# Optimization experiments

Hardware: AMD Instinct MI355X
Metric: run time of the kernel (lower is better)

The kernel has to match this reference:

```python
import jax, jax.numpy as jnp
import numpy as np

N_NODES = 50000
N_EDGES = 800000
IN_DIM = 256
NHID = 64
OUT_DIM = 64
DEPTH = 4
P = 2.0


def _gcn_conv(x, W, b, src, dst, n):
    # PyG GCNConv: xW, add self-loops, sym-normalize, aggregate src->dst, + bias
    xw = x @ W
    loop = jnp.arange(n)
    s = jnp.concatenate([src, loop])
    d = jnp.concatenate([dst, loop])
    deg = jax.ops.segment_sum(jnp.ones_like(d, dtype=xw.dtype), d, num_segments=n)
    dis = jnp.where(deg > 0, jax.lax.rsqrt(jnp.maximum(deg, 1.0)), 0.0)
    w = dis[s] * dis[d]  # [E+n]
    out = jax.ops.segment_sum(w[:, None] * xw[s], d, num_segments=n)
    return out + b


def _g2_gate(x, W, b, src, dst, n):
    xg = jax.nn.relu(_gcn_conv(x, W, b, src, dst, n))
    diff = jnp.abs(xg[src] - xg[dst]) ** P  # [E, nhid]
    sums = jax.ops.segment_sum(diff, src, num_segments=n)
    cnt = jax.ops.segment_sum(jnp.ones((src.shape[0],), dtype=x.dtype), src, num_segments=n)
    return jnp.tanh(sums / jnp.maximum(cnt, 1.0)[:, None])


def setup_inputs() -> dict:
    key = jax.random.key(0)
    ks = jax.random.split(key, 10)
    x = jax.random.normal(ks[0], (N_NODES, IN_DIM), dtype=jnp.float32)
    edge_index = jax.random.randint(ks[1], (2, N_EDGES), 0, N_NODES, dtype=jnp.int64 if jax.config.jax_enable_x64 else jnp.int32)
    s = 0.05
    return {
        "x": x,
        "edge_index": edge_index,
        "enc_w": jax.random.normal(ks[2], (IN_DIM, NHID), dtype=jnp.float32) * s,
        "enc_b": jnp.zeros((NHID,), dtype=jnp.float32),
        "conv_w": jax.random.normal(ks[3], (NHID, NHID), dtype=jnp.float32) * s,
        "conv_b": jnp.zeros((NHID,), dtype=jnp.float32),
        "gg_w": jax.random.normal(ks[4], (NHID, NHID), dtype=jnp.float32) * s,
        "gg_b": jnp.zeros((NHID,), dtype=jnp.float32),
        "dec_w": jax.random.normal(ks[5], (NHID, OUT_DIM), dtype=jnp.float32) * s,
        "dec_b": jnp.zeros((OUT_DIM,), dtype=jnp.float32),
    }


def reference(x, edge_index, enc_w, enc_b, conv_w, conv_b, gg_w, gg_b, dec_w, dec_b):
    n = x.shape[0]
    src, dst = edge_index[0], edge_index[1]
    # eval mode: dropouts are identity
    X = jax.nn.relu(x @ enc_w + enc_b)
    for _ in range(DEPTH):
        X_ = jax.nn.relu(_gcn_conv(X, conv_w, conv_b, src, dst, n))
        tau = _g2_gate(X, gg_w, gg_b, src, dst, n)
        X = (1.0 - tau) * X + tau * X_
    X = jax.nn.relu(X @ dec_w + dec_b)
    return X
```

## Files before the change

### kernel.cpp

```cpp
#include <hip/hip_runtime.h>
#include <math.h>

#define NN 50000
#define NE 800000
#define IND 256
#define NH 64
#define DEPTH 4
#define PART_DIV 6250
#define SB 49


__device__ __forceinline__ unsigned short f2bf(float f) {
    unsigned int x = __float_as_uint(f);
    unsigned int r = (x + 0x7fffu + ((x >> 16) & 1u)) >> 16;
    return (unsigned short)r;
}
__device__ __forceinline__ unsigned int pack2bf(float lo, float hi) {
    return (unsigned int)f2bf(lo) | ((unsigned int)f2bf(hi) << 16);
}
__device__ __forceinline__ ushort4 f4_to_us4(float4 f) {
    ushort4 u;
    u.x = f2bf(f.x); u.y = f2bf(f.y); u.z = f2bf(f.z); u.w = f2bf(f.w);
    return u;
}
__device__ __forceinline__ void acc8(float* a, uint4 r) {
    a[0] += __uint_as_float(r.x << 16); a[1] += __uint_as_float(r.x & 0xffff0000u);
    a[2] += __uint_as_float(r.y << 16); a[3] += __uint_as_float(r.y & 0xffff0000u);
    a[4] += __uint_as_float(r.z << 16); a[5] += __uint_as_float(r.z & 0xffff0000u);
    a[6] += __uint_as_float(r.w << 16); a[7] += __uint_as_float(r.w & 0xffff0000u);
}
__device__ __forceinline__ void unpack8(float* a, uint4 r) {
    a[0] = __uint_as_float(r.x << 16); a[1] = __uint_as_float(r.x & 0xffff0000u);
    a[2] = __uint_as_float(r.y << 16); a[3] = __uint_as_float(r.y & 0xffff0000u);
    a[4] = __uint_as_float(r.z << 16); a[5] = __uint_as_float(r.z & 0xffff0000u);
    a[6] = __uint_as_float(r.w << 16); a[7] = __uint_as_float(r.w & 0xffff0000u);
}
__device__ __forceinline__ void accd8(float* a, const float* xg, uint4 r) {
    float e;
    e = xg[0] - __uint_as_float(r.x << 16);         a[0] += e * e;
    e = xg[1] - __uint_as_float(r.x & 0xffff0000u); a[1] += e * e;
    e = xg[2] - __uint_as_float(r.y << 16);         a[2] += e * e;
    e = xg[3] - __uint_as_float(r.y & 0xffff0000u); a[3] += e * e;
    e = xg[4] - __uint_as_float(r.z << 16);         a[4] += e * e;
    e = xg[5] - __uint_as_float(r.z & 0xffff0000u); a[5] += e * e;
    e = xg[6] - __uint_as_float(r.w << 16);         a[6] += e * e;
    e = xg[7] - __uint_as_float(r.w & 0xffff0000u); a[7] += e * e;
}
__device__ __forceinline__ float tanh_pos(float x) {
    float t = __expf(-2.f * x);
    return (1.f - t) / (1.f + t);
}


__global__ void count_deg_rank(const int* __restrict__ src, const int* __restrict__ dst,
                               int* __restrict__ degin, int* __restrict__ degout,
                               int* __restrict__ rank_in, int* __restrict__ rank_out) {
    int e = blockIdx.x * blockDim.x + threadIdx.x;
    if (e < NE) {
        int s = src[e], d = dst[e];
        rank_in[e]  = atomicAdd(&degin[d], 1);
        rank_out[e] = atomicAdd(&degout[s], 1);
    }
}

__global__ __launch_bounds__(512) void scan_p1(const int* __restrict__ in0,
                                               const int* __restrict__ in1,
                                               int* __restrict__ tmp,
                                               int* __restrict__ bsum) {
    int a = blockIdx.x / SB;
    int b = blockIdx.x % SB;
    const int* in = a ? in1 : in0;
    int t = threadIdx.x;
    int base = b * 1024 + t * 2;
    int v0 = (base < NN) ? in[base] : 0;
    int v1 = (base + 1 < NN) ? in[base + 1] : 0;
    int v = v0 + v1;
    int x = v;
#pragma unroll
    for (int off = 1; off < 64; off <<= 1) {
        int u = __shfl_up(x, off);
        if ((t & 63) >= off) x += u;
    }
    __shared__ int ws[8];
    int wid = t >> 6, lane = t & 63;
    if (lane == 63) ws[wid] = x;
    __syncthreads();
    if (t == 0) {
        int run = 0;
#pragma unroll
        for (int w = 0; w < 8; ++w) { int s = ws[w]; ws[w] = run; run += s; }
    }
    __syncthreads();
    x += ws[wid];
    int excl = x - v;
    if (base < NN) tmp[a * NN + base] = excl;
    if (base + 1 < NN) tmp[a * NN + base + 1] = excl + v0;
    if (t == 511) bsum[a * SB + b] = x;
}

__global__ __launch_bounds__(128) void scan_p2(int* __restrict__ bsum,
                                               int* __restrict__ out0,
                                               int* __restrict__ out1) {
    int t = threadIdx.x;
    int a = t >> 6, lane = t & 63;
    int v = (lane < SB) ? bsum[a * SB + lane] : 0;
    int x = v;
#pragma unroll
    for (int off = 1; off < 64; off <<= 1) {
        int u = __shfl_up(x, off);
        if (lane >= off) x += u;
    }
    if (lane < SB) bsum[a * SB + lane] = x - v;
    if (lane == SB - 1) {
        if (a == 0) out0[NN] = x; else out1[NN] = x;
    }
}

__global__ __launch_bounds__(512) void scan_p3(const int* __restrict__ tmp,
                                               const int* __restrict__ bsum,
                                               int* __restrict__ out0,
                                               int* __restrict__ out1) {
    int a = blockIdx.x / SB;
    int b = blockIdx.x % SB;
    int* out = a ? out1 : out0;
    int add = bsum[a * SB + b];
    int t = threadIdx.x;
    int base = b * 1024 + t * 2;
    if (base < NN) out[base] = tmp[a * NN + base] + add;
    if (base + 1 < NN) out[base + 1] = tmp[a * NN + base + 1] + add;
}

__global__ void init_node(const int* __restrict__ degin, const int* __restrict__ degout,
                          float* __restrict__ dis, float* __restrict__ cntf) {
    int i = blockIdx.x * blockDim.x + threadIdx.x;
    if (i < NN) {
        dis[i] = rsqrtf((float)(degin[i] + 1));
        int od = degout[i];
        cntf[i] = (float)(od > 0 ? od : 1);
    }
}

__global__ void fill_csr_part(const int* __restrict__ src, const int* __restrict__ dst,
                              const int* __restrict__ off_dst, const int* __restrict__ off_src,
                              const int* __restrict__ rank_in, const int* __restrict__ rank_out,
                              int* __restrict__ srcs_by_dst, int* __restrict__ dsts_by_src,
                              int nGroups) {
    int p = blockIdx.x & 7;
    int g = blockIdx.x >> 3;
    for (int e = g * 256 + threadIdx.x; e < NE; e += nGroups * 256) {
        int s = src[e], d = dst[e];
        if (d / PART_DIV == p) srcs_by_dst[off_dst[d] + rank_in[e]] = s;
        if (s / PART_DIV == p) dsts_by_src[off_src[s] + rank_out[e]] = d;
    }
}

template<int K, bool RELU, bool WSC>
__global__ __launch_bounds__(256) void gemm64b(const float* __restrict__ X,
                                               const float* __restrict__ W,
                                               const float* __restrict__ bias,
                                               const float* __restrict__ rowscale,
                                               float* __restrict__ out,
                                               unsigned short* __restrict__ xsc, int n) {
    __shared__ float Ws[64 * 64];
    __shared__ float Xs[64][68];
    int tid = threadIdx.x;
    int row0 = blockIdx.x * 64;
    int r16 = tid >> 4;
    int cg = tid & 15;
    float4 acc[4];
#pragma unroll
    for (int t = 0; t < 4; ++t) acc[t] = make_float4(0.f, 0.f, 0.f, 0.f);

    for (int kc = 0; kc < K; kc += 64) {
        const float4* W4 = (const float4*)(W + (size_t)kc * 64);
        float4* Ws4 = (float4*)Ws;
#pragma unroll
        for (int t = 0; t < 4; ++t) Ws4[tid + t * 256] = W4[tid + t * 256];
#pragma unroll
        for (int t = 0; t < 4; ++t) {
            int r = r16 + t * 16;
            int grow = row0 + r;
            float4 xv = make_float4(0.f, 0.f, 0.f, 0.f);
            if (grow < n) xv = *(const float4*)(X + (size_t)grow * K + kc + cg * 4);
            Xs[r][cg * 4 + 0] = xv.x; Xs[r][cg * 4 + 1] = xv.y;
            Xs[r][cg * 4 + 2] = xv.z; Xs[r][cg * 4 + 3] = xv.w;
        }
        __syncthreads();
#pragma unroll
        for (int k = 0; k < 64; ++k) {
            float4 w4 = ((const float4*)Ws)[k * 16 + cg];
#pragma unroll
            for (int t = 0; t < 4; ++t) {
                float xv = Xs[r16 + t * 16][k];
                acc[t].x += xv * w4.x; acc[t].y += xv * w4.y;
                acc[t].z += xv * w4.z; acc[t].w += xv * w4.w;
            }
        }
        __syncthreads();
    }

    float4 b4 = ((const float4*)bias)[cg];
#pragma unroll
    for (int t = 0; t < 4; ++t) {
        int row = row0 + r16 + t * 16;
        if (row < n) {
            float4 o;
            o.x = acc[t].x + b4.x; o.y = acc[t].y + b4.y;
            o.z = acc[t].z + b4.z; o.w = acc[t].w + b4.w;
            if (RELU) {
                o.x = fmaxf(o.x, 0.f); o.y = fmaxf(o.y, 0.f);
                o.z = fmaxf(o.z, 0.f); o.w = fmaxf(o.w, 0.f);
            }
            ((float4*)(out + (size_t)row * 64))[cg] = o;
            if (WSC) {
                float s = rowscale[row];
                float4 o2 = make_float4(o.x * s, o.y * s, o.z * s, o.w * s);
                ((ushort4*)(xsc + (size_t)row * 64))[cg] = f4_to_us4(o2);
            }
        }
    }
}

template<bool OUTBF>
__global__ __launch_bounds__(256) void gemm64z(const float* __restrict__ Z,
                                               const float* __restrict__ W,
                                               const float* __restrict__ bias,
                                               float* __restrict__ outf,
                                               unsigned short* __restrict__ outb, int n) {
    __shared__ float Ws[64 * 64];
    __shared__ float Xs[64][68];
    int tid = threadIdx.x;
    int row0 = blockIdx.x * 64;
    int r16 = tid >> 4;
    int cg = tid & 15;
    float4 acc[4];
#pragma unroll
    for (int t = 0; t < 4; ++t) acc[t] = make_float4(0.f, 0.f, 0.f, 0.f);

    {
        const float4* W4 = (const float4*)W;
        float4* Ws4 = (float4*)Ws;
#pragma unroll
        for (int t = 0; t < 4; ++t) Ws4[tid + t * 256] = W4[tid + t * 256];
#pragma unroll
        for (int t = 0; t < 4; ++t) {
            int r = r16 + t * 16;
            int gr = row0 + r;
            float4 xv = make_float4(0.f, 0.f, 0.f, 0.f);
            if (gr < n) xv = *(const float4*)(Z + (size_t)gr * 64 + cg * 4);
            Xs[r][cg * 4 + 0] = xv.x; Xs[r][cg * 4 + 1] = xv.y;
            Xs[r][cg * 4 + 2] = xv.z; Xs[r][cg * 4 + 3] = xv.w;
        }
        __syncthreads();
#pragma unroll
        for (int k = 0; k < 64; ++k) {
            float4 w4 = ((const float4*)Ws)[k * 16 + cg];
#pragma unroll
            for (int t = 0; t < 4; ++t) {
                float xv = Xs[r16 + t * 16][k];
                acc[t].x += xv * w4.x; acc[t].y += xv * w4.y;
                acc[t].z += xv * w4.z; acc[t].w += xv * w4.w;
            }
        }
    }

    float4 b4 = ((const float4*)bias)[cg];
#pragma unroll
    for (int t = 0; t < 4; ++t) {
        int row = row0 + r16 + t * 16;
        if (row < n) {
            float4 o;
            o.x = fmaxf(acc[t].x + b4.x, 0.f); o.y = fmaxf(acc[t].y + b4.y, 0.f);
            o.z = fmaxf(acc[t].z + b4.z, 0.f); o.w = fmaxf(acc[t].w + b4.w, 0.f);
            if (OUTBF) {
                ((ushort4*)(outb + (size_t)row * 64))[cg] = f4_to_us4(o);
            } else {
                ((float4*)(outf + (size_t)row * 64))[cg] = o;
            }
        }
    }
}

__global__ __launch_bounds__(256) void zgather(
    const unsigned short* __restrict__ Xbf,
    const int* __restrict__ off, const int* __restrict__ nbr,
    const float* __restrict__ dis, float* __restrict__ Z)
{
    int t = blockIdx.x * 256 + threadIdx.x;
    int node = t >> 3, l8 = t & 7;
    if (node >= NN) return;
    const uint4* Xb = (const uint4*)Xbf;
    float a[8];
    unpack8(a, Xb[(size_t)node * 8 + l8]);
    int lo = off[node], hi = off[node + 1];
    int j = lo;
    for (; j + 7 < hi; j += 8) {
        int s0 = nbr[j],     s1 = nbr[j + 1], s2 = nbr[j + 2], s3 = nbr[j + 3];
        int s4 = nbr[j + 4], s5 = nbr[j + 5], s6 = nbr[j + 6], s7 = nbr[j + 7];
        uint4 r0 = Xb[(size_t)s0 * 8 + l8];
        uint4 r1 = Xb[(size_t)s1 * 8 + l8];
        uint4 r2 = Xb[(size_t)s2 * 8 + l8];
        uint4 r3 = Xb[(size_t)s3 * 8 + l8];
        uint4 r4 = Xb[(size_t)s4 * 8 + l8];
        uint4 r5 = Xb[(size_t)s5 * 8 + l8];
        uint4 r6 = Xb[(size_t)s6 * 8 + l8];
        uint4 r7 = Xb[(size_t)s7 * 8 + l8];
        acc8(a, r0); acc8(a, r1); acc8(a, r2); acc8(a, r3);
        acc8(a, r4); acc8(a, r5); acc8(a, r6); acc8(a, r7);
    }
    for (; j + 3 < hi; j += 4) {
        int s0 = nbr[j], s1 = nbr[j + 1], s2 = nbr[j + 2], s3 = nbr[j + 3];
        uint4 r0 = Xb[(size_t)s0 * 8 + l8];
        uint4 r1 = Xb[(size_t)s1 * 8 + l8];
        uint4 r2 = Xb[(size_t)s2 * 8 + l8];
        uint4 r3 = Xb[(size_t)s3 * 8 + l8];
        acc8(a, r0); acc8(a, r1); acc8(a, r2); acc8(a, r3);
    }
    for (; j < hi; ++j) {
        acc8(a, Xb[(size_t)nbr[j] * 8 + l8]);
    }
    float di = dis[node];
    float* zp = Z + (size_t)node * 64 + l8 * 8;
    *(float4*)(zp)     = make_float4(di * a[0], di * a[1], di * a[2], di * a[3]);
    *(float4*)(zp + 4) = make_float4(di * a[4], di * a[5], di * a[6], di * a[7]);
}

__global__ __launch_bounds__(256) void gate_update8(
    const unsigned short* __restrict__ Cbf, const float* __restrict__ Xn,
    float* __restrict__ X, unsigned short* __restrict__ Xbf,
    const int* __restrict__ off, const int* __restrict__ nbr,
    const float* __restrict__ cntf, const float* __restrict__ dis)
{
    int t = blockIdx.x * 256 + threadIdx.x;
    int node = t >> 3, l8 = t & 7;
    if (node >= NN) return;
    const uint4* Cb = (const uint4*)Cbf;
    float xg[8];
    unpack8(xg, Cb[(size_t)node * 8 + l8]);
    float a[8] = {0.f, 0.f, 0.f, 0.f, 0.f, 0.f, 0.f, 0.f};
    int lo = off[node], hi = off[node + 1];
    int j = lo;
    for (; j + 7 < hi; j += 8) {
        int d0 = nbr[j],     d1 = nbr[j + 1], d2 = nbr[j + 2], d3 = nbr[j + 3];
        int d4 = nbr[j + 4], d5 = nbr[j + 5], d6 = nbr[j + 6], d7 = nbr[j + 7];
        uint4 r0 = Cb[(size_t)d0 * 8 + l8];
        uint4 r1 = Cb[(size_t)d1 * 8 + l8];
        uint4 r2 = Cb[(size_t)d2 * 8 + l8];
        uint4 r3 = Cb[(size_t)d3 * 8 + l8];
        uint4 r4 = Cb[(size_t)d4 * 8 + l8];
        uint4 r5 = Cb[(size_t)d5 * 8 + l8];
        uint4 r6 = Cb[(size_t)d6 * 8 + l8];
        uint4 r7 = Cb[(size_t)d7 * 8 + l8];
        accd8(a, xg, r0); accd8(a, xg, r1); accd8(a, xg, r2); accd8(a, xg, r3);
        accd8(a, xg, r4); accd8(a, xg, r5); accd8(a, xg, r6); accd8(a, xg, r7);
    }
    for (; j + 3 < hi; j += 4) {
        int d0 = nbr[j], d1 = nbr[j + 1], d2 = nbr[j + 2], d3 = nbr[j + 3];
        uint4 r0 = Cb[(size_t)d0 * 8 + l8];
        uint4 r1 = Cb[(size_t)d1 * 8 + l8];
        uint4 r2 = Cb[(size_t)d2 * 8 + l8];
        uint4 r3 = Cb[(size_t)d3 * 8 + l8];
        accd8(a, xg, r0); accd8(a, xg, r1); accd8(a, xg, r2); accd8(a, xg, r3);
    }
    for (; j < hi; ++j) {
        accd8(a, xg, Cb[(size_t)nbr[j] * 8 + l8]);
    }
    float inv = 1.f / cntf[node];
    float di = dis[node];
    const float* xop = X + (size_t)node * 64 + l8 * 8;
    const float* xnp = Xn + (size_t)node * 64 + l8 * 8;
    float o[8];
#pragma unroll
    for (int k = 0; k < 8; ++k) {
        float tau = tanh_pos(a[k] * inv);
        float xo = xop[k], xn = xnp[k];
        o[k] = xo + tau * (xn - xo);
    }
    float* xp = X + (size_t)node * 64 + l8 * 8;
    *(float4*)(xp)     = make_float4(o[0], o[1], o[2], o[3]);
    *(float4*)(xp + 4) = make_float4(o[4], o[5], o[6], o[7]);
    uint4 pk;
    pk.x = pack2bf(o[0] * di, o[1] * di);
    pk.y = pack2bf(o[2] * di, o[3] * di);
    pk.z = pack2bf(o[4] * di, o[5] * di);
    pk.w = pack2bf(o[6] * di, o[7] * di);
    ((uint4*)Xbf)[(size_t)node * 8 + l8] = pk;
}


extern "C" void kernel_launch(void* const* d_in, const int* in_sizes, int n_in,
                              void* d_out, int out_size, void* d_ws, size_t ws_size,
                              hipStream_t stream) {
    const float* x      = (const float*)d_in[0];
    const int*   ei     = (const int*)d_in[1];
    const float* enc_w  = (const float*)d_in[2];
    const float* enc_b  = (const float*)d_in[3];
    const float* conv_w = (const float*)d_in[4];
    const float* conv_b = (const float*)d_in[5];
    const float* gg_w   = (const float*)d_in[6];
    const float* gg_b   = (const float*)d_in[7];
    const float* dec_w  = (const float*)d_in[8];
    const float* dec_b  = (const float*)d_in[9];
    float* out = (float*)d_out;

    const int* src = ei;
    const int* dst = ei + NE;

    char* p = (char*)d_ws;
    auto alloc = [&](size_t bytes) -> void* {
        void* r = (void*)p;
        p += (bytes + 255) & ~(size_t)255;
        return r;
    };
    float* X   = (float*)alloc((size_t)NN * 64 * 4);
    float* Zb  = (float*)alloc((size_t)NN * 64 * 4);
    float* B   = (float*)alloc((size_t)NN * 64 * 4);
    unsigned short* Xbf = (unsigned short*)alloc((size_t)NN * 64 * 2);
    unsigned short* Cbf = (unsigned short*)alloc((size_t)NN * 64 * 2);
    float* dis  = (float*)alloc((size_t)NN * 4);
    float* cntf = (float*)alloc((size_t)NN * 4);
    int* degin   = (int*)alloc((size_t)NN * 4);
    int* degout  = (int*)alloc((size_t)NN * 4);
    int* off_dst = (int*)alloc((size_t)(NN + 1) * 4);
    int* off_src = (int*)alloc((size_t)(NN + 1) * 4);
    int* rank_in  = (int*)alloc((size_t)NE * 4);
    int* rank_out = (int*)alloc((size_t)NE * 4);
    int* sbd     = (int*)alloc((size_t)NE * 4);
    int* dbs     = (int*)alloc((size_t)NE * 4);
    int* stmp    = (int*)alloc((size_t)2 * NN * 4);
    int* bsum    = (int*)alloc((size_t)2 * SB * 4);

    hipMemsetAsync(degin, 0, (size_t)NN * 4, stream);
    hipMemsetAsync(degout, 0, (size_t)NN * 4, stream);

    const int EB = (NE + 255) / 256;
    const int NB = (NN + 255) / 256;
    const int NGROUPS = 104;
    count_deg_rank<<<EB, 256, 0, stream>>>(src, dst, degin, degout, rank_in, rank_out);
    scan_p1<<<2 * SB, 512, 0, stream>>>(degin, degout, stmp, bsum);
    scan_p2<<<1, 128, 0, stream>>>(bsum, off_dst, off_src);
    scan_p3<<<2 * SB, 512, 0, stream>>>(stmp, bsum, off_dst, off_src);
    init_node<<<NB, 256, 0, stream>>>(degin, degout, dis, cntf);
    fill_csr_part<<<8 * NGROUPS, 256, 0, stream>>>(src, dst, off_dst, off_src,
                                                   rank_in, rank_out, sbd, dbs, NGROUPS);

    const int GB = (NN + 63) / 64;
    const int OB = ((NN * 8) + 255) / 256;

    gemm64b<IND, true, true><<<GB, 256, 0, stream>>>(x, enc_w, enc_b, dis, X, Xbf, NN);

    for (int l = 0; l < DEPTH; ++l) {
        zgather<<<OB, 256, 0, stream>>>(Xbf, off_dst, sbd, dis, Zb);
        gemm64z<false><<<GB, 256, 0, stream>>>(Zb, conv_w, conv_b, B, nullptr, NN);
        gemm64z<true><<<GB, 256, 0, stream>>>(Zb, gg_w, gg_b, nullptr, Cbf, NN);
        gate_update8<<<OB, 256, 0, stream>>>(Cbf, B, X, Xbf, off_src, dbs, cntf, dis);
    }

    gemm64b<NH, true, false><<<GB, 256, 0, stream>>>(X, dec_w, dec_b, nullptr, out, nullptr, NN);
}
```

Before: 680.1 us.

## Privatize degree histograms per edge partition and shuffle-broadcast neighbor indices

Degree counting now uses eight per-partition histograms, one for each contiguous slice of edges. A reduce pass turns them into per-partition prefix offsets, and the CSR fill combines those offsets with local ranks. The aim is to spread out atomic contention, presumably per XCD, and to keep histogram traffic local. Separately, the gather kernels load neighbor indices once per lane and broadcast them with __shfl instead of having each of the 8 lanes load all 8 indices. This adds a reduce kernel, 3.2 MB of histogram memsets, and an fill_csr_part that loops over all eight partitions.

Result: no change. 685.2 us (+0.7%).

```diff
diff --git a/kernel.cpp b/kernel.cpp
--- a/kernel.cpp
+++ b/kernel.cpp
@@ -8,6 +8,7 @@
 #define DEPTH 4
 #define PART_DIV 6250
 #define SB 49
+#define EPP 100000
 
 
 __device__ __forceinline__ unsigned short f2bf(float f) {
@@ -52,15 +53,38 @@
 }
 
 
-__global__ void count_deg_rank(const int* __restrict__ src, const int* __restrict__ dst,
-                               int* __restrict__ degin, int* __restrict__ degout,
-                               int* __restrict__ rank_in, int* __restrict__ rank_out) {
-    int e = blockIdx.x * blockDim.x + threadIdx.x;
-    if (e < NE) {
+__global__ void count8(const int* __restrict__ src, const int* __restrict__ dst,
+                       int* __restrict__ hin, int* __restrict__ hout,
+                       int* __restrict__ lrin, int* __restrict__ lrout,
+                       int nGroups) {
+    int p = blockIdx.x & 7;
+    int g = blockIdx.x >> 3;
+    int* hi = hin + p * NN;
+    int* ho = hout + p * NN;
+    for (int i = g * 256 + threadIdx.x; i < EPP; i += nGroups * 256) {
+        int e = p * EPP + i;
         int s = src[e], d = dst[e];
-        rank_in[e]  = atomicAdd(&degin[d], 1);
-        rank_out[e] = atomicAdd(&degout[s], 1);
-    }
+        lrin[e]  = atomicAdd(&hi[d], 1);
+        lrout[e] = atomicAdd(&ho[s], 1);
+    }
+}
+
+__global__ void reduce8(int* __restrict__ hin, int* __restrict__ hout,
+                        int* __restrict__ degin, int* __restrict__ degout) {
+    int i = blockIdx.x * blockDim.x + threadIdx.x;
+    if (i >= NN) return;
+    int run = 0;
+#pragma unroll
+    for (int p = 0; p < 8; ++p) {
+        int t = hin[p * NN + i]; hin[p * NN + i] = run; run += t;
+    }
+    degin[i] = run;
+    run = 0;
+#pragma unroll
+    for (int p = 0; p < 8; ++p) {
+        int t = hout[p * NN + i]; hout[p * NN + i] = run; run += t;
+    }
+    degout[i] = run;
 }
 
 __global__ __launch_bounds__(512) void scan_p1(const int* __restrict__ in0,
@@ -142,15 +166,21 @@
 
 __global__ void fill_csr_part(const int* __restrict__ src, const int* __restrict__ dst,
                               const int* __restrict__ off_dst, const int* __restrict__ off_src,
-                              const int* __restrict__ rank_in, const int* __restrict__ rank_out,
+                              const int* __restrict__ hin, const int* __restrict__ hout,
+                              const int* __restrict__ lrin, const int* __restrict__ lrout,
                               int* __restrict__ srcs_by_dst, int* __restrict__ dsts_by_src,
                               int nGroups) {
-    int p = blockIdx.x & 7;
+    int q = blockIdx.x & 7;
     int g = blockIdx.x >> 3;
-    for (int e = g * 256 + threadIdx.x; e < NE; e += nGroups * 256) {
-        int s = src[e], d = dst[e];
-        if (d / PART_DIV == p) srcs_by_dst[off_dst[d] + rank_in[e]] = s;
-        if (s / PART_DIV == p) dsts_by_src[off_src[s] + rank_out[e]] = d;
+    for (int pe = 0; pe < 8; ++pe) {
+        const int* bin = hin + pe * NN;
+        const int* bout = hout + pe * NN;
+        for (int i = g * 256 + threadIdx.x; i < EPP; i += nGroups * 256) {
+            int e = pe * EPP + i;
+            int s = src[e], d = dst[e];
+            if (d / PART_DIV == q) srcs_by_dst[off_dst[d] + bin[d] + lrin[e]] = s;
+            if (s / PART_DIV == q) dsts_by_src[off_src[s] + bout[s] + lrout[e]] = d;
+        }
     }
 }
 
@@ -289,14 +319,19 @@
     int t = blockIdx.x * 256 + threadIdx.x;
     int node = t >> 3, l8 = t & 7;
     if (node >= NN) return;
+    int lane = threadIdx.x & 63;
+    int octbase = lane & ~7;
     const uint4* Xb = (const uint4*)Xbf;
     float a[8];
     unpack8(a, Xb[(size_t)node * 8 + l8]);
     int lo = off[node], hi = off[node + 1];
     int j = lo;
     for (; j + 7 < hi; j += 8) {
-        int s0 = nbr[j],     s1 = nbr[j + 1], s2 = nbr[j + 2], s3 = nbr[j + 3];
-        int s4 = nbr[j + 4], s5 = nbr[j + 5], s6 = nbr[j + 6], s7 = nbr[j + 7];
+        int nv = nbr[j + l8];
+        int s0 = __shfl(nv, octbase + 0), s1 = __shfl(nv, octbase + 1);
+        int s2 = __shfl(nv, octbase + 2), s3 = __shfl(nv, octbase + 3);
+        int s4 = __shfl(nv, octbase + 4), s5 = __shfl(nv, octbase + 5);
+        int s6 = __shfl(nv, octbase + 6), s7 = __shfl(nv, octbase + 7);
         uint4 r0 = Xb[(size_t)s0 * 8 + l8];
         uint4 r1 = Xb[(size_t)s1 * 8 + l8];
         uint4 r2 = Xb[(size_t)s2 * 8 + l8];
@@ -334,6 +369,8 @@
     int t = blockIdx.x * 256 + threadIdx.x;
     int node = t >> 3, l8 = t & 7;
     if (node >= NN) return;
+    int lane = threadIdx.x & 63;
+    int octbase = lane & ~7;
     const uint4* Cb = (const uint4*)Cbf;
     float xg[8];
     unpack8(xg, Cb[(size_t)node * 8 + l8]);
@@ -341,8 +378,11 @@
     int lo = off[node], hi = off[node + 1];
     int j = lo;
     for (; j + 7 < hi; j += 8) {
-        int d0 = nbr[j],     d1 = nbr[j + 1], d2 = nbr[j + 2], d3 = nbr[j + 3];
-        int d4 = nbr[j + 4], d5 = nbr[j + 5], d6 = nbr[j + 6], d7 = nbr[j + 7];
+        int nv = nbr[j + l8];
+        int d0 = __shfl(nv, octbase + 0), d1 = __shfl(nv, octbase + 1);
+        int d2 = __shfl(nv, octbase + 2), d3 = __shfl(nv, octbase + 3);
+        int d4 = __shfl(nv, octbase + 4), d5 = __shfl(nv, octbase + 5);
+        int d6 = __shfl(nv, octbase + 6), d7 = __shfl(nv, octbase + 7);
         uint4 r0 = Cb[(size_t)d0 * 8 + l8];
         uint4 r1 = Cb[(size_t)d1 * 8 + l8];
         uint4 r2 = Cb[(size_t)d2 * 8 + l8];
@@ -423,26 +463,29 @@
     int* degout  = (int*)alloc((size_t)NN * 4);
     int* off_dst = (int*)alloc((size_t)(NN + 1) * 4);
     int* off_src = (int*)alloc((size_t)(NN + 1) * 4);
-    int* rank_in  = (int*)alloc((size_t)NE * 4);
-    int* rank_out = (int*)alloc((size_t)NE * 4);
+    int* hin     = (int*)alloc((size_t)8 * NN * 4);
+    int* hout    = (int*)alloc((size_t)8 * NN * 4);
+    int* lrin    = (int*)alloc((size_t)NE * 4);
+    int* lrout   = (int*)alloc((size_t)NE * 4);
     int* sbd     = (int*)alloc((size_t)NE * 4);
     int* dbs     = (int*)alloc((size_t)NE * 4);
     int* stmp    = (int*)alloc((size_t)2 * NN * 4);
     int* bsum    = (int*)alloc((size_t)2 * SB * 4);
 
-    hipMemsetAsync(degin, 0, (size_t)NN * 4, stream);
-    hipMemsetAsync(degout, 0, (size_t)NN * 4, stream);
-
-    const int EB = (NE + 255) / 256;
+    hipMemsetAsync(hin, 0, (size_t)8 * NN * 4, stream);
+    hipMemsetAsync(hout, 0, (size_t)8 * NN * 4, stream);
+
     const int NB = (NN + 255) / 256;
     const int NGROUPS = 104;
-    count_deg_rank<<<EB, 256, 0, stream>>>(src, dst, degin, degout, rank_in, rank_out);
+    count8<<<8 * NGROUPS, 256, 0, stream>>>(src, dst, hin, hout, lrin, lrout, NGROUPS);
+    reduce8<<<NB, 256, 0, stream>>>(hin, hout, degin, degout);
     scan_p1<<<2 * SB, 512, 0, stream>>>(degin, degout, stmp, bsum);
     scan_p2<<<1, 128, 0, stream>>>(bsum, off_dst, off_src);
     scan_p3<<<2 * SB, 512, 0, stream>>>(stmp, bsum, off_dst, off_src);
     init_node<<<NB, 256, 0, stream>>>(degin, degout, dis, cntf);
     fill_csr_part<<<8 * NGROUPS, 256, 0, stream>>>(src, dst, off_dst, off_src,
-                                                   rank_in, rank_out, sbd, dbs, NGROUPS);
+                                                   hin, hout, lrin, lrout,
+                                                   sbd, dbs, NGROUPS);
 
     const int GB = (NN + 63) / 64;
     const int OB = ((NN * 8) + 255) / 256;
```
